# Kernel optimization log

Hardware: AMD Instinct MI355X
Metric: run time of the kernel (lower is better)

Reference implementation:

```python
import jax, jax.numpy as jnp
import numpy as np

B, S, D, H, INNER = 2, 2048, 1024, 16, 4096
HD = D // H
EPS = 1e-5


def setup_inputs() -> dict:
    key = jax.random.key(0)
    ks = jax.random.split(key, 8)

    def w(k, o, i):
        return jax.random.normal(k, (o, i), jnp.float32) * 0.02

    return {
        "hidden_states": jax.random.normal(ks[0], (B, S, D), jnp.float32),
        "attention_mask": jnp.ones((B, S), jnp.float32),
        "wq": w(ks[1], D, D), "bq": jnp.zeros((D,), jnp.float32),
        "wk": w(ks[2], D, D), "bk": jnp.zeros((D,), jnp.float32),
        "wv": w(ks[3], D, D), "bv": jnp.zeros((D,), jnp.float32),
        "wo": w(ks[4], D, D), "bo": jnp.zeros((D,), jnp.float32),
        "w1": w(ks[5], INNER, D), "b1": jnp.zeros((INNER,), jnp.float32),
        "w2": w(ks[6], D, INNER), "b2": jnp.zeros((D,), jnp.float32),
        "g1": jnp.ones((D,), jnp.float32), "be1": jnp.zeros((D,), jnp.float32),
        "g2": jnp.ones((D,), jnp.float32), "be2": jnp.zeros((D,), jnp.float32),
        "w_bits": 8,
        "a_bits": 8,
    }


def fake_quant(x, bits):
    # symmetric per-tensor fake quantization with straight-through estimator
    qmax = 2.0 ** (bits - 1) - 1.0
    scale = jnp.maximum(jnp.max(jnp.abs(x)), 1e-8) / qmax
    q = jnp.round(jnp.clip(x / scale, -qmax, qmax)) * scale
    return x + jax.lax.stop_gradient(q - x)


def qlinear(x, w, b, w_bits, a_bits):
    return fake_quant(x, a_bits) @ fake_quant(w, w_bits).T + b


def layernorm(x, g, b):
    m = jnp.mean(x, axis=-1, keepdims=True)
    v = jnp.mean((x - m) ** 2, axis=-1, keepdims=True)
    return (x - m) * jax.lax.rsqrt(v + EPS) * g + b


def reference(hidden_states, attention_mask, wq, bq, wk, bk, wv, bv, wo, bo,
              w1, b1, w2, b2, g1, be1, g2, be2, w_bits, a_bits):
    # --- attention sub-block ---
    residual = hidden_states
    x = layernorm(hidden_states, g1, be1)
    q = qlinear(x, wq, bq, w_bits, a_bits).reshape(B, S, H, HD)
    k = qlinear(x, wk, bk, w_bits, a_bits).reshape(B, S, H, HD)
    v = qlinear(x, wv, bv, w_bits, a_bits).reshape(B, S, H, HD)
    scores = jnp.einsum("bqhd,bkhd->bhqk", q, k) / jnp.sqrt(jnp.float32(HD))
    scores = scores + (1.0 - attention_mask)[:, None, None, :] * -10000.0
    probs = jax.nn.softmax(scores, axis=-1)
    attn = jnp.einsum("bhqk,bkhd->bqhd", probs, v).reshape(B, S, D)
    attn = qlinear(attn, wo, bo, w_bits, a_bits)
    hidden = residual + attn
    # --- MLP sub-block ---
    residual = hidden
    x = layernorm(hidden, g2, be2)
    x = qlinear(x, w1, b1, w_bits, a_bits)
    x = jax.nn.gelu(x, approximate=False)
    x = qlinear(x, w2, b2, w_bits, a_bits)
    return residual + x
```

## Files before the change

### kernel.cpp

```cpp
#include <hip/hip_runtime.h>
#include <hip/hip_bf16.h>
#include <math.h>

typedef __bf16 bf16;
typedef __bf16 bf16x8 __attribute__((ext_vector_type(8)));
typedef __bf16 bf16x4 __attribute__((ext_vector_type(4)));
typedef float  f32x4  __attribute__((ext_vector_type(4)));
typedef float  f32x16 __attribute__((ext_vector_type(16)));
typedef unsigned int u32x4 __attribute__((ext_vector_type(4)));

static constexpr int B_  = 2;
static constexpr int S_  = 2048;
static constexpr int D_  = 1024;
static constexpr int H_  = 16;
static constexpr int HD_ = 64;
static constexpr int I_  = 4096;
static constexpr int NT  = B_ * S_;

__device__ __forceinline__ void atomicMaxF(float* p, float v) {
  atomicMax((unsigned int*)p, __float_as_uint(v));
}

__device__ __forceinline__ f32x4 mfma16(bf16x8 a, bf16x8 b, f32x4 c) {
  return __builtin_amdgcn_mfma_f32_16x16x32_bf16(a, b, c, 0, 0, 0);
}

__device__ __forceinline__ f32x16 mfma32(bf16x8 a, bf16x8 b, f32x16 c) {
  return __builtin_amdgcn_mfma_f32_32x32x16_bf16(a, b, c, 0, 0, 0);
}

__device__ __forceinline__ void gload16(const void* g, void* lds) {
  __builtin_amdgcn_global_load_lds(
      (const __attribute__((address_space(1))) void*)g,
      (__attribute__((address_space(3))) void*)lds, 16, 0, 0);
}

__device__ __forceinline__ float quant1(float x, float scale, float qmax) {
  return rintf(fminf(fmaxf(x / scale, -qmax), qmax)) * scale;
}

__device__ __forceinline__ void stage64b(const bf16* __restrict__ g, int rs, bf16* lds, int t) {
  #pragma unroll
  for (int r = 0; r < 4; r++) {
    const int cl  = r * 128 + t;
    const int row = cl >> 3;
    const int scr = (cl & 7) ^ (row & 7);
    gload16(g + (size_t)row * rs + scr * 8,
            (char*)lds + (size_t)(r * 128 + (t & 64)) * 16);
  }
}

__global__ __launch_bounds__(256) void k_prep(const float* __restrict__ mask,
                                              float* __restrict__ madd, float* __restrict__ scal) {
  constexpr float MSK2 = -14426.950408889634f;
  const int i = blockIdx.x * 256 + threadIdx.x;
  if (blockIdx.x == 0 && threadIdx.x < 32) scal[threadIdx.x] = 0.f;
  if (i < B_ * S_) madd[i] = (1.0f - mask[i]) * MSK2;
}

struct WArgs {
  const float* w[6];
  bf16* q[6];
  size_t n4[6];
};

__global__ __launch_bounds__(256) void k_absmax6(WArgs a, float* __restrict__ slots) {
  const int z = blockIdx.z;
  const float* __restrict__ x = a.w[z];
  const size_t n4 = a.n4[z];
  size_t i = (size_t)blockIdx.x * 256 + threadIdx.x;
  const size_t stride = (size_t)gridDim.x * 256;
  float m = 0.f;
  for (; i < n4; i += stride) {
    float4 v = ((const float4*)x)[i];
    m = fmaxf(m, fmaxf(fmaxf(fabsf(v.x), fabsf(v.y)), fmaxf(fabsf(v.z), fabsf(v.w))));
  }
  #pragma unroll
  for (int o = 32; o; o >>= 1) m = fmaxf(m, __shfl_xor(m, o));
  __shared__ float red[4];
  if ((threadIdx.x & 63) == 0) red[threadIdx.x >> 6] = m;
  __syncthreads();
  if (threadIdx.x == 0)
    atomicMaxF(slots + z, fmaxf(fmaxf(red[0], red[1]), fmaxf(red[2], red[3])));
}

__global__ __launch_bounds__(256) void k_quant6(WArgs a, const float* __restrict__ slots,
                                                const int* __restrict__ bits) {
  const int z = blockIdx.z;
  const float* __restrict__ x = a.w[z];
  bf16* __restrict__ y = a.q[z];
  const size_t n4 = a.n4[z];
  const float qmax  = (float)((1 << (*bits - 1)) - 1);
  const float scale = fmaxf(slots[z], 1e-8f) / qmax;
  size_t i = (size_t)blockIdx.x * 256 + threadIdx.x;
  const size_t stride = (size_t)gridDim.x * 256;
  for (; i < n4; i += stride) {
    float4 v = ((const float4*)x)[i];
    bf16x4 o;
    o[0] = (bf16)quant1(v.x, scale, qmax);
    o[1] = (bf16)quant1(v.y, scale, qmax);
    o[2] = (bf16)quant1(v.z, scale, qmax);
    o[3] = (bf16)quant1(v.w, scale, qmax);
    ((bf16x4*)y)[i] = o;
  }
}

__global__ __launch_bounds__(256) void k_quant(const float* __restrict__ x, bf16* __restrict__ y,
                                               const float* __restrict__ slot,
                                               const int* __restrict__ bits, size_t n4) {
  const float qmax  = (float)((1 << (*bits - 1)) - 1);
  const float scale = fmaxf(*slot, 1e-8f) / qmax;
  size_t i = (size_t)blockIdx.x * 256 + threadIdx.x;
  const size_t stride = (size_t)gridDim.x * 256;
  for (; i < n4; i += stride) {
    float4 v = ((const float4*)x)[i];
    bf16x4 o;
    o[0] = (bf16)quant1(v.x, scale, qmax);
    o[1] = (bf16)quant1(v.y, scale, qmax);
    o[2] = (bf16)quant1(v.z, scale, qmax);
    o[3] = (bf16)quant1(v.w, scale, qmax);
    ((bf16x4*)y)[i] = o;
  }
}

__global__ __launch_bounds__(256) void k_quant_ip(bf16* __restrict__ x,
                                                  const float* __restrict__ slot,
                                                  const int* __restrict__ bits, size_t n8) {
  const float qmax  = (float)((1 << (*bits - 1)) - 1);
  const float scale = fmaxf(*slot, 1e-8f) / qmax;
  size_t i = (size_t)blockIdx.x * 256 + threadIdx.x;
  if (i >= n8) return;
  bf16x8 v = ((const bf16x8*)x)[i];
  #pragma unroll
  for (int j = 0; j < 8; j++) v[j] = (bf16)quant1((float)v[j], scale, qmax);
  ((bf16x8*)x)[i] = v;
}

__global__ __launch_bounds__(256) void k_ln(const float* __restrict__ x, const float* __restrict__ g,
                                            const float* __restrict__ be, float* __restrict__ y,
                                            float* __restrict__ slot) {
  const int row = blockIdx.x, t = threadIdx.x;
  const float4 v = ((const float4*)(x + (size_t)row * D_))[t];
  float s = v.x + v.y + v.z + v.w;
  float q = v.x * v.x + v.y * v.y + v.z * v.z + v.w * v.w;
  #pragma unroll
  for (int o = 32; o; o >>= 1) { s += __shfl_xor(s, o); q += __shfl_xor(q, o); }
  __shared__ float red[8];
  const int wid = t >> 6;
  if ((t & 63) == 0) { red[wid] = s; red[4 + wid] = q; }
  __syncthreads();
  s = red[0] + red[1] + red[2] + red[3];
  q = red[4] + red[5] + red[6] + red[7];
  const float mean = s * (1.f / D_);
  const float rstd = rsqrtf(q * (1.f / D_) - mean * mean + 1e-5f);
  const float4 gv = ((const float4*)g)[t];
  const float4 bv = ((const float4*)be)[t];
  float4 o;
  o.x = (v.x - mean) * rstd * gv.x + bv.x;
  o.y = (v.y - mean) * rstd * gv.y + bv.y;
  o.z = (v.z - mean) * rstd * gv.z + bv.z;
  o.w = (v.w - mean) * rstd * gv.w + bv.w;
  ((float4*)(y + (size_t)row * D_))[t] = o;
  float m = fmaxf(fmaxf(fabsf(o.x), fabsf(o.y)), fmaxf(fabsf(o.z), fabsf(o.w)));
  #pragma unroll
  for (int oo = 32; oo; oo >>= 1) m = fmaxf(m, __shfl_xor(m, oo));
  __syncthreads();
  if ((t & 63) == 0) red[wid] = m;
  __syncthreads();
  if (t == 0) atomicMaxF(slot, fmaxf(fmaxf(red[0], red[1]), fmaxf(red[2], red[3])));
}

struct GemmArgs {
  const bf16* A;
  const bf16* B0; const bf16* B1; const bf16* B2;
  const float* bias0; const float* bias1; const float* bias2;
  void* out0; void* out1; void* out2;
  const float* res;
  float* slot;
  int K; int ldc;
};

template <int MODE, int MT>
__device__ __forceinline__ void gemm_body(GemmArgs a, int bx, int by, int bz) {
  constexpr int TM = MT * 32;
  __shared__ __align__(16) bf16 As[2][TM * 64];
  __shared__ __align__(16) bf16 Bs[2][128 * 64];
  const int t = threadIdx.x, wid = t >> 6, lane = t & 63;
  const int grp = lane >> 4, l15 = lane & 15;
  const int wm = wid >> 1, wn = wid & 1;
  const size_t m0 = (size_t)bx * TM, n0 = (size_t)by * 128;
  const int K = a.K, ldc = a.ldc;

  const bf16* Bw; const float* bias; void* outv;
  if constexpr (MODE == 0) {
    Bw   = bz == 0 ? a.B0 : (bz == 1 ? a.B1 : a.B2);
    bias = bz == 0 ? a.bias0 : (bz == 1 ? a.bias1 : a.bias2);
    outv = bz == 0 ? a.out0 : (bz == 1 ? a.out1 : a.out2);
  } else {
    Bw = a.B0; bias = a.bias0; outv = a.out0;
  }

  const f32x4 zero = {0.f, 0.f, 0.f, 0.f};
  f32x4 acc[MT][4];
  #pragma unroll
  for (int m = 0; m < MT; m++)
    #pragma unroll
    for (int n = 0; n < 4; n++) acc[m][n] = zero;

  auto stage = [&](int kt, int buf) {
    #pragma unroll
    for (int r = 0; r < MT; r++) {
      const int cl = r * 256 + t;
      const int row = cl >> 3, c = cl & 7;
      gload16(a.A + (m0 + row) * (size_t)K + kt + ((c ^ (row & 7)) * 8),
              (char*)&As[buf][0] + (size_t)(r * 256 + (t & 192)) * 16);
    }
    #pragma unroll
    for (int r = 0; r < 4; r++) {
      const int cl = r * 256 + t;
      const int row = cl >> 3, c = cl & 7;
      gload16(Bw + (n0 + row) * (size_t)K + kt + ((c ^ (row & 7)) * 8),
              (char*)&Bs[buf][0] + (size_t)(r * 256 + (t & 192)) * 16);
    }
  };

  stage(0, 0);
  __syncthreads();
  int cur = 0;
  for (int kt = 0; kt < K; kt += 64) {
    if (kt + 64 < K) stage(kt + 64, cur ^ 1);
    #pragma unroll
    for (int ks = 0; ks < 2; ks++) {
      bf16x8 bfv[4];
      #pragma unroll
      for (int n = 0; n < 4; n++) {
        const int rb = wn * 64 + n * 16 + l15;
        bfv[n] = *(const bf16x8*)(&Bs[cur][0] + rb * 64 + (((ks * 4 + grp) ^ (rb & 7)) * 8));
      }
      #pragma unroll
      for (int m = 0; m < MT; m++) {
        const int ra = wm * (MT * 16) + m * 16 + l15;
        const bf16x8 af = *(const bf16x8*)(&As[cur][0] + ra * 64 + (((ks * 4 + grp) ^ (ra & 7)) * 8));
        #pragma unroll
        for (int n = 0; n < 4; n++)
          acc[m][n] = mfma16(af, bfv[n], acc[m][n]);
      }
    }
    __syncthreads();
    cur ^= 1;
  }

  const size_t gr0 = m0 + wm * (MT * 16) + grp * 4;
  const size_t gc0 = n0 + wn * 64 + l15;

  if constexpr (MODE == 0) {
    if (bz == 2) {
      #pragma unroll
      for (int n = 0; n < 4; n++) {
        const size_t gc = gc0 + n * 16;
        const float bc = bias[gc];
        #pragma unroll
        for (int m = 0; m < MT; m++) {
          const size_t gr = gr0 + m * 16;
          const size_t bb = gr >> 11, s0 = gr & (S_ - 1);
          bf16x4 vv;
          #pragma unroll
          for (int i = 0; i < 4; i++) vv[i] = (bf16)(acc[m][n][i] + bc);
          *(bf16x4*)((bf16*)outv + bb * (size_t)D_ * S_ + gc * S_ + s0) = vv;
        }
      }
      return;
    }
  }

  float lmax = 0.f;
  #pragma unroll
  for (int n = 0; n < 4; n++) {
    const size_t gc = gc0 + n * 16;
    const float bc = bias[gc];
    #pragma unroll
    for (int m = 0; m < MT; m++) {
      const size_t gr = gr0 + m * 16;
      #pragma unroll
      for (int i = 0; i < 4; i++) {
        const float v = acc[m][n][i] + bc;
        const size_t idx = (gr + i) * (size_t)ldc + gc;
        if constexpr (MODE == 0) {
          ((bf16*)outv)[idx] = (bf16)v;
        } else if constexpr (MODE == 1) {
          ((float*)outv)[idx] = v + a.res[idx];
        } else {
          const float gl = 0.5f * v * (1.0f + erff(v * 0.7071067811865475f));
          ((bf16*)outv)[idx] = (bf16)gl;
          lmax = fmaxf(lmax, fabsf(gl));
        }
      }
    }
  }
  if constexpr (MODE == 2) {
    #pragma unroll
    for (int o = 32; o; o >>= 1) lmax = fmaxf(lmax, __shfl_xor(lmax, o));
    float* red = (float*)&As[0][0];
    if (lane == 0) red[wid] = lmax;
    __syncthreads();
    if (t == 0) atomicMaxF(a.slot, fmaxf(fmaxf(red[0], red[1]), fmaxf(red[2], red[3])));
  }
}

__global__ __launch_bounds__(256) void k_gqkv(GemmArgs a) {
  const int d = blockIdx.x, c = d & 7, s = d >> 3;
  gemm_body<0, 4>(a, s / 3, c, s % 3);
}
__global__ __launch_bounds__(256) void k_gout(GemmArgs a) {
  const int d = blockIdx.x, c = d & 7, s = d >> 3;
  gemm_body<1, 2>(a, s, c, 0);
}
__global__ __launch_bounds__(256) void k_gmlp1(GemmArgs a) {
  const int d = blockIdx.x, c = d & 7, s = d >> 3;
  gemm_body<2, 4>(a, s >> 2, c * 4 + (s & 3), 0);
}
__global__ __launch_bounds__(256) void k_gmlp2(GemmArgs a) {
  const int d = blockIdx.x, c = d & 7, s = d >> 3;
  gemm_body<1, 2>(a, ((c >> 2) << 5) | (s >> 1), ((c & 3) << 1) | (s & 1), 0);
}

__global__ __launch_bounds__(128) void k_attn(const bf16* __restrict__ qb, const bf16* __restrict__ kb,
                                              const bf16* __restrict__ vt, const float* __restrict__ madd,
                                              float* __restrict__ out, float* __restrict__ slot) {
  constexpr float SCL2 = 0.18033688011112042f;
  constexpr float THR  = 8.0f;
  __shared__ __align__(16) bf16 Ks[2][64 * 64];
  __shared__ __align__(16) bf16 Vs[2][64 * 64];
  __shared__ float red[2];
  const int t = threadIdx.x, wid = t >> 6, lane = t & 63;
  const int l31 = lane & 31, hi = lane >> 5;
  const int b = blockIdx.y >> 4, h = blockIdx.y & 15;
  const size_t qkbase = ((size_t)b * S_) * D_ + (size_t)h * HD_;
  const size_t vtbase = (size_t)b * D_ * S_ + (size_t)h * HD_ * S_;
  const int q = blockIdx.x * 64 + wid * 32 + l31;

  bf16x8 qf[4];
  #pragma unroll
  for (int j = 0; j < 4; j++)
    qf[j] = *(const bf16x8*)(qb + qkbase + (size_t)q * D_ + j * 16 + hi * 8);

  f32x16 ao0, ao1;
  #pragma unroll
  for (int r = 0; r < 16; r++) { ao0[r] = 0.f; ao1[r] = 0.f; }
  float mi = -INFINITY, li = 0.f;

  stage64b(kb + qkbase, D_, Ks[0], t);
  stage64b(vt + vtbase, S_, Vs[0], t);
  __syncthreads();
  int cur = 0;

  const float* mp = madd + (size_t)b * S_ + hi * 4;

  for (int kt0 = 0; kt0 < S_; kt0 += 64) {
    f32x4 mv[2][4];
    #pragma unroll
    for (int kb2 = 0; kb2 < 2; kb2++)
      #pragma unroll
      for (int g = 0; g < 4; g++)
        mv[kb2][g] = *(const f32x4*)(mp + kt0 + kb2 * 32 + g * 8);
    __builtin_amdgcn_sched_barrier(0);
    if (kt0 + 64 < S_) {
      stage64b(kb + qkbase + (size_t)(kt0 + 64) * D_, D_, Ks[cur ^ 1], t);
      stage64b(vt + vtbase + (kt0 + 64), S_, Vs[cur ^ 1], t);
    }

    f32x16 s0, s1;
    #pragma unroll
    for (int r = 0; r < 16; r++) { s0[r] = 0.f; s1[r] = 0.f; }
    #pragma unroll
    for (int j = 0; j < 4; j++) {
      const int ch = (j * 2 + hi);
      const bf16x8 kf0 = *(const bf16x8*)(&Ks[cur][0] + l31 * 64 + ((ch ^ (l31 & 7)) * 8));
      const bf16x8 kf1 = *(const bf16x8*)(&Ks[cur][0] + (32 + l31) * 64 + ((ch ^ (l31 & 7)) * 8));
      s0 = mfma32(kf0, qf[j], s0);
      s1 = mfma32(kf1, qf[j], s1);
    }

    float pv_[32];
    #pragma unroll
    for (int r = 0; r < 16; r++) pv_[r]      = s0[r] * SCL2 + mv[0][r >> 2][r & 3];
    #pragma unroll
    for (int r = 0; r < 16; r++) pv_[16 + r] = s1[r] * SCL2 + mv[1][r >> 2][r & 3];

    float mx = pv_[0];
    #pragma unroll
    for (int r = 1; r < 32; r++) mx = fmaxf(mx, pv_[r]);
    mx = fmaxf(mx, __shfl_xor(mx, 32));

    if (!__all(mx - mi <= THR)) {
      const float mnew = fmaxf(mi, mx);
      const float co = exp2f(mi - mnew);
      li *= co;
      #pragma unroll
      for (int r = 0; r < 16; r++) { ao0[r] *= co; ao1[r] *= co; }
      mi = mnew;
    }

    float ls = 0.f;
    #pragma unroll
    for (int r = 0; r < 32; r++) { pv_[r] = exp2f(pv_[r] - mi); ls += pv_[r]; }
    li += ls;

    unsigned pk[16];
    #pragma unroll
    for (int tt = 0; tt < 8; tt++) {
      asm("v_cvt_pk_bf16_f32 %0, %1, %2" : "=v"(pk[tt])     : "v"(pv_[2 * tt]),      "v"(pv_[2 * tt + 1]));
      asm("v_cvt_pk_bf16_f32 %0, %1, %2" : "=v"(pk[8 + tt]) : "v"(pv_[16 + 2 * tt]), "v"(pv_[16 + 2 * tt + 1]));
    }
    #pragma unroll
    for (int g = 0; g < 4; g++) {
      asm volatile("v_permlane32_swap_b32 %0, %1" : "+v"(pk[4 * g]),     "+v"(pk[4 * g + 2]));
      asm volatile("v_permlane32_swap_b32 %0, %1" : "+v"(pk[4 * g + 1]), "+v"(pk[4 * g + 3]));
    }

    #pragma unroll
    for (int j = 0; j < 4; j++) {
      const u32x4 w = {pk[4 * j], pk[4 * j + 1], pk[4 * j + 2], pk[4 * j + 3]};
      const bf16x8 pf = __builtin_bit_cast(bf16x8, w);
      const int ch = (j * 2 + hi);
      const bf16x8 vf0 = *(const bf16x8*)(&Vs[cur][0] + l31 * 64 + ((ch ^ (l31 & 7)) * 8));
      const bf16x8 vf1 = *(const bf16x8*)(&Vs[cur][0] + (32 + l31) * 64 + ((ch ^ (l31 & 7)) * 8));
      ao0 = mfma32(vf0, pf, ao0);
      ao1 = mfma32(vf1, pf, ao1);
    }
    __syncthreads();
    cur ^= 1;
  }

  li += __shfl_xor(li, 32);
  const float invl = 1.0f / li;
  float lmax = 0.f;
  float* orow = out + qkbase + (size_t)q * D_;
  #pragma unroll
  for (int db2 = 0; db2 < 2; db2++) {
    #pragma unroll
    for (int rg = 0; rg < 4; rg++) {
      float4 o;
      o.x = (db2 ? ao1[rg * 4 + 0] : ao0[rg * 4 + 0]) * invl;
      o.y = (db2 ? ao1[rg * 4 + 1] : ao0[rg * 4 + 1]) * invl;
      o.z = (db2 ? ao1[rg * 4 + 2] : ao0[rg * 4 + 2]) * invl;
      o.w = (db2 ? ao1[rg * 4 + 3] : ao0[rg * 4 + 3]) * invl;
      *(float4*)(orow + db2 * 32 + rg * 8 + hi * 4) = o;
      lmax = fmaxf(lmax, fmaxf(fmaxf(fabsf(o.x), fabsf(o.y)), fmaxf(fabsf(o.z), fabsf(o.w))));
    }
  }
  #pragma unroll
  for (int o = 32; o; o >>= 1) lmax = fmaxf(lmax, __shfl_xor(lmax, o));
  if (lane == 0) red[wid] = lmax;
  __syncthreads();
  if (t == 0) atomicMaxF(slot, fmaxf(red[0], red[1]));
}

extern "C" void kernel_launch(void* const* d_in, const int* in_sizes, int n_in,
                              void* d_out, int out_size, void* d_ws, size_t ws_size,
                              hipStream_t stream) {
  const float* hs   = (const float*)d_in[0];
  const float* mask = (const float*)d_in[1];
  const float* wq = (const float*)d_in[2];  const float* bq = (const float*)d_in[3];
  const float* wk = (const float*)d_in[4];  const float* bk = (const float*)d_in[5];
  const float* wv = (const float*)d_in[6];  const float* bv = (const float*)d_in[7];
  const float* wo = (const float*)d_in[8];  const float* bo = (const float*)d_in[9];
  const float* w1 = (const float*)d_in[10]; const float* b1 = (const float*)d_in[11];
  const float* w2 = (const float*)d_in[12]; const float* b2 = (const float*)d_in[13];
  const float* g1 = (const float*)d_in[14]; const float* be1 = (const float*)d_in[15];
  const float* g2 = (const float*)d_in[16]; const float* be2 = (const float*)d_in[17];
  const int* wbits = (const int*)d_in[18];
  const int* abits = (const int*)d_in[19];

  char* ws = (char*)d_ws;
  size_t off = 0;
  float* scal = (float*)ws;                      off += 256;
  float* maddg= (float*)(ws + off);              off += (size_t)NT * 4;
  float* fbuf = (float*)(ws + off);              off += (size_t)NT * D_ * 4;
  bf16*  qx   = (bf16*)(ws + off);               off += (size_t)NT * D_ * 2;
  bf16*  qb   = (bf16*)(ws + off);               off += (size_t)NT * D_ * 2;
  bf16*  kbuf = (bf16*)(ws + off);               off += (size_t)NT * D_ * 2;
  bf16*  vbuf = (bf16*)(ws + off);               off += (size_t)NT * D_ * 2;
  float* h2   = (float*)(ws + off);              off += (size_t)NT * D_ * 4;
  bf16*  h1   = (bf16*)(ws + off);               off += (size_t)NT * I_ * 2;
  bf16*  wqq  = (bf16*)(ws + off);               off += (size_t)D_ * D_ * 2;
  bf16*  wkq  = (bf16*)(ws + off);               off += (size_t)D_ * D_ * 2;
  bf16*  wvq  = (bf16*)(ws + off);               off += (size_t)D_ * D_ * 2;
  bf16*  woq  = (bf16*)(ws + off);               off += (size_t)D_ * D_ * 2;
  bf16*  w1q  = (bf16*)(ws + off);               off += (size_t)I_ * D_ * 2;
  bf16*  w2q  = (bf16*)(ws + off);               off += (size_t)D_ * I_ * 2;
  if (ws_size < off) return;

  k_prep<<<NT / 256, 256, 0, stream>>>(mask, maddg, scal);

  const size_t nDD4 = (size_t)D_ * D_ / 4, nDI4 = (size_t)D_ * I_ / 4;
  WArgs wa;
  wa.w[0] = wq; wa.w[1] = wk; wa.w[2] = wv; wa.w[3] = wo; wa.w[4] = w1; wa.w[5] = w2;
  wa.q[0] = wqq; wa.q[1] = wkq; wa.q[2] = wvq; wa.q[3] = woq; wa.q[4] = w1q; wa.q[5] = w2q;
  wa.n4[0] = nDD4; wa.n4[1] = nDD4; wa.n4[2] = nDD4; wa.n4[3] = nDD4;
  wa.n4[4] = nDI4; wa.n4[5] = nDI4;
  k_absmax6<<<dim3(1024, 1, 6), 256, 0, stream>>>(wa, scal + 4);
  k_quant6<<<dim3(1024, 1, 6), 256, 0, stream>>>(wa, scal + 4, wbits);

  const size_t nND4 = (size_t)NT * D_ / 4;

  k_ln<<<NT, 256, 0, stream>>>(hs, g1, be1, fbuf, scal + 0);
  k_quant<<<2048, 256, 0, stream>>>(fbuf, qx, scal + 0, abits, nND4);
  {
    GemmArgs ga{};
    ga.A = qx; ga.B0 = wqq; ga.B1 = wkq; ga.B2 = wvq;
    ga.bias0 = bq; ga.bias1 = bk; ga.bias2 = bv;
    ga.out0 = qb; ga.out1 = kbuf; ga.out2 = vbuf;
    ga.K = D_; ga.ldc = D_;
    k_gqkv<<<(NT / 128) * (D_ / 128) * 3, 256, 0, stream>>>(ga);
  }

  k_attn<<<dim3(S_ / 64, B_ * H_), 128, 0, stream>>>(qb, kbuf, vbuf, maddg, fbuf, scal + 1);
  k_quant<<<2048, 256, 0, stream>>>(fbuf, qx, scal + 1, abits, nND4);
  {
    GemmArgs ga{};
    ga.A = qx; ga.B0 = woq; ga.bias0 = bo; ga.out0 = h2; ga.res = hs;
    ga.K = D_; ga.ldc = D_;
    k_gout<<<(NT / 64) * (D_ / 128), 256, 0, stream>>>(ga);
  }

  k_ln<<<NT, 256, 0, stream>>>(h2, g2, be2, fbuf, scal + 2);
  k_quant<<<2048, 256, 0, stream>>>(fbuf, qx, scal + 2, abits, nND4);
  {
    GemmArgs ga{};
    ga.A = qx; ga.B0 = w1q; ga.bias0 = b1; ga.out0 = h1; ga.slot = scal + 3;
    ga.K = D_; ga.ldc = I_;
    k_gmlp1<<<(NT / 128) * (I_ / 128), 256, 0, stream>>>(ga);
  }
  k_quant_ip<<<(NT * (size_t)I_ / 8 + 255) / 256, 256, 0, stream>>>(h1, scal + 3, abits,
                                                                    (size_t)NT * I_ / 8);
  {
    GemmArgs ga{};
    ga.A = h1; ga.B0 = w2q; ga.bias0 = b2; ga.out0 = d_out; ga.res = h2;
    ga.K = I_; ga.ldc = D_;
    k_gmlp2<<<(NT / 64) * (D_ / 128), 256, 0, stream>>>(ga);
  }
}
```

Before: 488.0 us.

## Run quantized GEMMs as int8 MFMA with integer codes and fused rescale

Weights and activations are now stored as int8 quantization codes instead of bf16 dequantized values. All four GEMM variants use the 16x16x64 i8 MFMA with int32 accumulation, a 128-wide K step and the same LDS tile footprint, then apply scale_a*scale_w in the epilogue. This halves operand memory traffic and gives roughly twice the MFMA throughput. It relies on the codes being exact integers within int8 range, which holds only when bits<=8.

```diff
diff --git a/kernel.cpp b/kernel.cpp
--- a/kernel.cpp
+++ b/kernel.cpp
@@ -3,8 +3,12 @@
 #include <math.h>
 
 typedef __bf16 bf16;
+typedef signed char i8;
 typedef __bf16 bf16x8 __attribute__((ext_vector_type(8)));
 typedef __bf16 bf16x4 __attribute__((ext_vector_type(4)));
+typedef signed char i8x4 __attribute__((ext_vector_type(4)));
+typedef signed char i8x8 __attribute__((ext_vector_type(8)));
+typedef int    i32x4 __attribute__((ext_vector_type(4)));
 typedef float  f32x4  __attribute__((ext_vector_type(4)));
 typedef float  f32x16 __attribute__((ext_vector_type(16)));
 typedef unsigned int u32x4 __attribute__((ext_vector_type(4)));
@@ -21,12 +25,12 @@
   atomicMax((unsigned int*)p, __float_as_uint(v));
 }
 
-__device__ __forceinline__ f32x4 mfma16(bf16x8 a, bf16x8 b, f32x4 c) {
-  return __builtin_amdgcn_mfma_f32_16x16x32_bf16(a, b, c, 0, 0, 0);
-}
-
 __device__ __forceinline__ f32x16 mfma32(bf16x8 a, bf16x8 b, f32x16 c) {
   return __builtin_amdgcn_mfma_f32_32x32x16_bf16(a, b, c, 0, 0, 0);
+}
+
+__device__ __forceinline__ i32x4 mfma_i8(i32x4 a, i32x4 b, i32x4 c) {
+  return __builtin_amdgcn_mfma_i32_16x16x64_i8(a, b, c, 0, 0, 0);
 }
 
 __device__ __forceinline__ void gload16(const void* g, void* lds) {
@@ -37,6 +41,9 @@
 
 __device__ __forceinline__ float quant1(float x, float scale, float qmax) {
   return rintf(fminf(fmaxf(x / scale, -qmax), qmax)) * scale;
+}
+__device__ __forceinline__ i8 quantn(float x, float scale, float qmax) {
+  return (i8)(int)rintf(fminf(fmaxf(x / scale, -qmax), qmax));
 }
 
 __device__ __forceinline__ void stage64b(const bf16* __restrict__ g, int rs, bf16* lds, int t) {
@@ -60,7 +67,7 @@
 
 struct WArgs {
   const float* w[6];
-  bf16* q[6];
+  i8* q[6];
   size_t n4[6];
 };
 
@@ -88,7 +95,7 @@
                                                 const int* __restrict__ bits) {
   const int z = blockIdx.z;
   const float* __restrict__ x = a.w[z];
-  bf16* __restrict__ y = a.q[z];
+  i8* __restrict__ y = a.q[z];
   const size_t n4 = a.n4[z];
   const float qmax  = (float)((1 << (*bits - 1)) - 1);
   const float scale = fmaxf(slots[z], 1e-8f) / qmax;
@@ -96,16 +103,16 @@
   const size_t stride = (size_t)gridDim.x * 256;
   for (; i < n4; i += stride) {
     float4 v = ((const float4*)x)[i];
-    bf16x4 o;
-    o[0] = (bf16)quant1(v.x, scale, qmax);
-    o[1] = (bf16)quant1(v.y, scale, qmax);
-    o[2] = (bf16)quant1(v.z, scale, qmax);
-    o[3] = (bf16)quant1(v.w, scale, qmax);
-    ((bf16x4*)y)[i] = o;
-  }
-}
-
-__global__ __launch_bounds__(256) void k_quant(const float* __restrict__ x, bf16* __restrict__ y,
+    i8x4 o;
+    o[0] = quantn(v.x, scale, qmax);
+    o[1] = quantn(v.y, scale, qmax);
+    o[2] = quantn(v.z, scale, qmax);
+    o[3] = quantn(v.w, scale, qmax);
+    ((i8x4*)y)[i] = o;
+  }
+}
+
+__global__ __launch_bounds__(256) void k_quant(const float* __restrict__ x, i8* __restrict__ y,
                                                const float* __restrict__ slot,
                                                const int* __restrict__ bits, size_t n4) {
   const float qmax  = (float)((1 << (*bits - 1)) - 1);
@@ -114,26 +121,27 @@
   const size_t stride = (size_t)gridDim.x * 256;
   for (; i < n4; i += stride) {
     float4 v = ((const float4*)x)[i];
-    bf16x4 o;
-    o[0] = (bf16)quant1(v.x, scale, qmax);
-    o[1] = (bf16)quant1(v.y, scale, qmax);
-    o[2] = (bf16)quant1(v.z, scale, qmax);
-    o[3] = (bf16)quant1(v.w, scale, qmax);
-    ((bf16x4*)y)[i] = o;
-  }
-}
-
-__global__ __launch_bounds__(256) void k_quant_ip(bf16* __restrict__ x,
-                                                  const float* __restrict__ slot,
-                                                  const int* __restrict__ bits, size_t n8) {
+    i8x4 o;
+    o[0] = quantn(v.x, scale, qmax);
+    o[1] = quantn(v.y, scale, qmax);
+    o[2] = quantn(v.z, scale, qmax);
+    o[3] = quantn(v.w, scale, qmax);
+    ((i8x4*)y)[i] = o;
+  }
+}
+
+__global__ __launch_bounds__(256) void k_qgelu(const bf16* __restrict__ x, i8* __restrict__ y,
+                                               const float* __restrict__ slot,
+                                               const int* __restrict__ bits, size_t n8) {
   const float qmax  = (float)((1 << (*bits - 1)) - 1);
   const float scale = fmaxf(*slot, 1e-8f) / qmax;
   size_t i = (size_t)blockIdx.x * 256 + threadIdx.x;
   if (i >= n8) return;
   bf16x8 v = ((const bf16x8*)x)[i];
-  #pragma unroll
-  for (int j = 0; j < 8; j++) v[j] = (bf16)quant1((float)v[j], scale, qmax);
-  ((bf16x8*)x)[i] = v;
+  i8x8 o;
+  #pragma unroll
+  for (int j = 0; j < 8; j++) o[j] = quantn((float)v[j], scale, qmax);
+  ((i8x8*)y)[i] = o;
 }
 
 __global__ __launch_bounds__(256) void k_ln(const float* __restrict__ x, const float* __restrict__ g,
@@ -171,55 +179,61 @@
 }
 
 struct GemmArgs {
-  const bf16* A;
-  const bf16* B0; const bf16* B1; const bf16* B2;
+  const i8* A;
+  const i8* B0; const i8* B1; const i8* B2;
   const float* bias0; const float* bias1; const float* bias2;
   void* out0; void* out1; void* out2;
   const float* res;
   float* slot;
+  const float* sa;
+  const float* sw0; const float* sw1; const float* sw2;
+  const int* abit; const int* wbit;
   int K; int ldc;
 };
 
 template <int MODE, int MT>
 __device__ __forceinline__ void gemm_body(GemmArgs a, int bx, int by, int bz) {
   constexpr int TM = MT * 32;
-  __shared__ __align__(16) bf16 As[2][TM * 64];
-  __shared__ __align__(16) bf16 Bs[2][128 * 64];
+  __shared__ __align__(16) i8 As[2][TM * 128];
+  __shared__ __align__(16) i8 Bs[2][128 * 128];
   const int t = threadIdx.x, wid = t >> 6, lane = t & 63;
   const int grp = lane >> 4, l15 = lane & 15;
   const int wm = wid >> 1, wn = wid & 1;
   const size_t m0 = (size_t)bx * TM, n0 = (size_t)by * 128;
   const int K = a.K, ldc = a.ldc;
 
-  const bf16* Bw; const float* bias; void* outv;
+  const i8* Bw; const float* bias; void* outv; const float* swp;
   if constexpr (MODE == 0) {
     Bw   = bz == 0 ? a.B0 : (bz == 1 ? a.B1 : a.B2);
     bias = bz == 0 ? a.bias0 : (bz == 1 ? a.bias1 : a.bias2);
     outv = bz == 0 ? a.out0 : (bz == 1 ? a.out1 : a.out2);
+    swp  = bz == 0 ? a.sw0 : (bz == 1 ? a.sw1 : a.sw2);
   } else {
-    Bw = a.B0; bias = a.bias0; outv = a.out0;
-  }
-
-  const f32x4 zero = {0.f, 0.f, 0.f, 0.f};
-  f32x4 acc[MT][4];
+    Bw = a.B0; bias = a.bias0; outv = a.out0; swp = a.sw0;
+  }
+  const float qa = (float)((1 << (*a.abit - 1)) - 1);
+  const float qw = (float)((1 << (*a.wbit - 1)) - 1);
+  const float sasw = (fmaxf(*a.sa, 1e-8f) / qa) * (fmaxf(*swp, 1e-8f) / qw);
+
+  i32x4 acc[MT][4];
   #pragma unroll
   for (int m = 0; m < MT; m++)
     #pragma unroll
-    for (int n = 0; n < 4; n++) acc[m][n] = zero;
+    for (int n = 0; n < 4; n++) acc[m][n] = i32x4{0, 0, 0, 0};
 
   auto stage = [&](int kt, int buf) {
     #pragma unroll
     for (int r = 0; r < MT; r++) {
       const int cl = r * 256 + t;
       const int row = cl >> 3, c = cl & 7;
-      gload16(a.A + (m0 + row) * (size_t)K + kt + ((c ^ (row & 7)) * 8),
+      gload16(a.A + (m0 + row) * (size_t)K + kt + ((c ^ (row & 7)) * 16),
               (char*)&As[buf][0] + (size_t)(r * 256 + (t & 192)) * 16);
     }
     #pragma unroll
     for (int r = 0; r < 4; r++) {
       const int cl = r * 256 + t;
       const int row = cl >> 3, c = cl & 7;
-      gload16(Bw + (n0 + row) * (size_t)K + kt + ((c ^ (row & 7)) * 8),
+      gload16(Bw + (n0 + row) * (size_t)K + kt + ((c ^ (row & 7)) * 16),
               (char*)&Bs[buf][0] + (size_t)(r * 256 + (t & 192)) * 16);
     }
   };
@@ -227,23 +241,23 @@
   stage(0, 0);
   __syncthreads();
   int cur = 0;
-  for (int kt = 0; kt < K; kt += 64) {
-    if (kt + 64 < K) stage(kt + 64, cur ^ 1);
+  for (int kt = 0; kt < K; kt += 128) {
+    if (kt + 128 < K) stage(kt + 128, cur ^ 1);
     #pragma unroll
     for (int ks = 0; ks < 2; ks++) {
-      bf16x8 bfv[4];
+      i32x4 bfv[4];
       #pragma unroll
       for (int n = 0; n < 4; n++) {
         const int rb = wn * 64 + n * 16 + l15;
-        bfv[n] = *(const bf16x8*)(&Bs[cur][0] + rb * 64 + (((ks * 4 + grp) ^ (rb & 7)) * 8));
+        bfv[n] = *(const i32x4*)(&Bs[cur][0] + rb * 128 + (((ks * 4 + grp) ^ (rb & 7)) * 16));
       }
       #pragma unroll
       for (int m = 0; m < MT; m++) {
         const int ra = wm * (MT * 16) + m * 16 + l15;
-        const bf16x8 af = *(const bf16x8*)(&As[cur][0] + ra * 64 + (((ks * 4 + grp) ^ (ra & 7)) * 8));
+        const i32x4 af = *(const i32x4*)(&As[cur][0] + ra * 128 + (((ks * 4 + grp) ^ (ra & 7)) * 16));
         #pragma unroll
         for (int n = 0; n < 4; n++)
-          acc[m][n] = mfma16(af, bfv[n], acc[m][n]);
+          acc[m][n] = mfma_i8(af, bfv[n], acc[m][n]);
       }
     }
     __syncthreads();
@@ -265,7 +279,7 @@
           const size_t bb = gr >> 11, s0 = gr & (S_ - 1);
           bf16x4 vv;
           #pragma unroll
-          for (int i = 0; i < 4; i++) vv[i] = (bf16)(acc[m][n][i] + bc);
+          for (int i = 0; i < 4; i++) vv[i] = (bf16)((float)acc[m][n][i] * sasw + bc);
           *(bf16x4*)((bf16*)outv + bb * (size_t)D_ * S_ + gc * S_ + s0) = vv;
         }
       }
@@ -283,7 +297,7 @@
       const size_t gr = gr0 + m * 16;
       #pragma unroll
       for (int i = 0; i < 4; i++) {
-        const float v = acc[m][n][i] + bc;
+        const float v = (float)acc[m][n][i] * sasw + bc;
         const size_t idx = (gr + i) * (size_t)ldc + gc;
         if constexpr (MODE == 0) {
           ((bf16*)outv)[idx] = (bf16)v;
@@ -477,18 +491,19 @@
   float* scal = (float*)ws;                      off += 256;
   float* maddg= (float*)(ws + off);              off += (size_t)NT * 4;
   float* fbuf = (float*)(ws + off);              off += (size_t)NT * D_ * 4;
-  bf16*  qx   = (bf16*)(ws + off);               off += (size_t)NT * D_ * 2;
+  i8*    qx   = (i8*)(ws + off);                 off += (size_t)NT * D_;
   bf16*  qb   = (bf16*)(ws + off);               off += (size_t)NT * D_ * 2;
   bf16*  kbuf = (bf16*)(ws + off);               off += (size_t)NT * D_ * 2;
   bf16*  vbuf = (bf16*)(ws + off);               off += (size_t)NT * D_ * 2;
   float* h2   = (float*)(ws + off);              off += (size_t)NT * D_ * 4;
   bf16*  h1   = (bf16*)(ws + off);               off += (size_t)NT * I_ * 2;
-  bf16*  wqq  = (bf16*)(ws + off);               off += (size_t)D_ * D_ * 2;
-  bf16*  wkq  = (bf16*)(ws + off);               off += (size_t)D_ * D_ * 2;
-  bf16*  wvq  = (bf16*)(ws + off);               off += (size_t)D_ * D_ * 2;
-  bf16*  woq  = (bf16*)(ws + off);               off += (size_t)D_ * D_ * 2;
-  bf16*  w1q  = (bf16*)(ws + off);               off += (size_t)I_ * D_ * 2;
-  bf16*  w2q  = (bf16*)(ws + off);               off += (size_t)D_ * I_ * 2;
+  i8*    h1q  = (i8*)(ws + off);                 off += (size_t)NT * I_;
+  i8*    wqq  = (i8*)(ws + off);                 off += (size_t)D_ * D_;
+  i8*    wkq  = (i8*)(ws + off);                 off += (size_t)D_ * D_;
+  i8*    wvq  = (i8*)(ws + off);                 off += (size_t)D_ * D_;
+  i8*    woq  = (i8*)(ws + off);                 off += (size_t)D_ * D_;
+  i8*    w1q  = (i8*)(ws + off);                 off += (size_t)I_ * D_;
+  i8*    w2q  = (i8*)(ws + off);                 off += (size_t)D_ * I_;
   if (ws_size < off) return;
 
   k_prep<<<NT / 256, 256, 0, stream>>>(mask, maddg, scal);
@@ -511,6 +526,8 @@
     ga.A = qx; ga.B0 = wqq; ga.B1 = wkq; ga.B2 = wvq;
     ga.bias0 = bq; ga.bias1 = bk; ga.bias2 = bv;
     ga.out0 = qb; ga.out1 = kbuf; ga.out2 = vbuf;
+    ga.sa = scal + 0; ga.sw0 = scal + 4; ga.sw1 = scal + 5; ga.sw2 = scal + 6;
+    ga.abit = abits; ga.wbit = wbits;
     ga.K = D_; ga.ldc = D_;
     k_gqkv<<<(NT / 128) * (D_ / 128) * 3, 256, 0, stream>>>(ga);
   }
@@ -520,6 +537,8 @@
   {
     GemmArgs ga{};
     ga.A = qx; ga.B0 = woq; ga.bias0 = bo; ga.out0 = h2; ga.res = hs;
+    ga.sa = scal + 1; ga.sw0 = scal + 7;
+    ga.abit = abits; ga.wbit = wbits;
     ga.K = D_; ga.ldc = D_;
     k_gout<<<(NT / 64) * (D_ / 128), 256, 0, stream>>>(ga);
   }
@@ -529,14 +548,18 @@
   {
     GemmArgs ga{};
     ga.A = qx; ga.B0 = w1q; ga.bias0 = b1; ga.out0 = h1; ga.slot = scal + 3;
+    ga.sa = scal + 2; ga.sw0 = scal + 8;
+    ga.abit = abits; ga.wbit = wbits;
     ga.K = D_; ga.ldc = I_;
     k_gmlp1<<<(NT / 128) * (I_ / 128), 256, 0, stream>>>(ga);
   }
-  k_quant_ip<<<(NT * (size_t)I_ / 8 + 255) / 256, 256, 0, stream>>>(h1, scal + 3, abits,
-                                                                    (size_t)NT * I_ / 8);
+  k_qgelu<<<(NT * (size_t)I_ / 8 + 255) / 256, 256, 0, stream>>>(h1, h1q, scal + 3, abits,
+                                                                 (size_t)NT * I_ / 8);
   {
     GemmArgs ga{};
-    ga.A = h1; ga.B0 = w2q; ga.bias0 = b2; ga.out0 = d_out; ga.res = h2;
+    ga.A = h1q; ga.B0 = w2q; ga.bias0 = b2; ga.out0 = d_out; ga.res = h2;
+    ga.sa = scal + 3; ga.sw0 = scal + 9;
+    ga.abit = abits; ga.wbit = wbits;
     ga.K = I_; ga.ldc = D_;
     k_gmlp2<<<(NT / 64) * (D_ / 128), 256, 0, stream>>>(ga);
   }
```

New measurement: 427.2 us. 1.14x faster.
